# Optimization experiments

Hardware: AMD Instinct MI355X
Metric: run time of the kernel (lower is better)

## Reference

```python
import jax, jax.numpy as jnp
import numpy as np

DIM = 1024
SEQ = 32768
BATCH = 1
MIN_ACTIVE = 0.01
MAX_ACTIVE = 0.1
KMAX = int(MAX_ACTIVE * DIM) + 1  # static upper bound on dynamic k (<= 102)
EPS = 1e-6


def setup_inputs() -> dict:
    key = jax.random.key(0)
    ks = jax.random.split(key, 7)
    h = DIM // 8
    s = 0.02
    return {
        "x": jax.random.normal(ks[0], (BATCH, SEQ, DIM), jnp.float32),
        # complexity_net: Linear(dim, dim//8) -> GELU -> Linear(dim//8, 1) -> Sigmoid
        "w1": jax.random.normal(ks[1], (DIM, h), jnp.float32) * s,
        "b1": jnp.zeros((h,), jnp.float32),
        "w2": jax.random.normal(ks[2], (h, 1), jnp.float32) * s,
        "b2": jnp.zeros((1,), jnp.float32),
        # gate_net: Linear(dim, dim)
        "wg": jax.random.normal(ks[3], (DIM, DIM), jnp.float32) * s,
        "bg": jnp.zeros((DIM,), jnp.float32),
        # running stats (eval mode: used for normalization, not updated)
        "running_mean": jax.random.normal(ks[4], (DIM,), jnp.float32) * 0.1,
        "running_var": jax.random.uniform(ks[5], (DIM,), jnp.float32, minval=0.5, maxval=1.5),
    }


def reference(x, w1, b1, w2, b2, wg, bg, running_mean, running_var):
    # complexity from seq-mean pooled features -> scalar in (0,1)
    pooled = x.mean(axis=1, keepdims=True)                      # (B,1,D)
    hid = jax.nn.gelu(pooled @ w1 + b1, approximate=False)      # torch GELU is exact erf
    complexity = jax.nn.sigmoid(hid @ w2 + b2)                  # (B,1,1)
    active_ratio = MIN_ACTIVE + (MAX_ACTIVE - MIN_ACTIVE) * complexity
    # torch .int() truncates; clamp(min=1). B==1 so k is effectively scalar.
    k = jnp.clip((active_ratio * DIM).astype(jnp.int32), 1, KMAX)  # (B,1,1)

    importance = jnp.abs(x @ wg + bg)                           # (B,S,D)
    importance = (importance - running_mean) / (jnp.sqrt(running_var) + EPS)

    # dynamic-k topk via static-KMAX top_k + threshold at the k-th largest value
    topk_vals, _ = jax.lax.top_k(importance, KMAX)              # (B,S,KMAX)
    idx = jnp.broadcast_to((k - 1).astype(jnp.int32), (x.shape[0], x.shape[1], 1))
    kth = jnp.take_along_axis(topk_vals, idx, axis=-1)          # (B,S,1)
    mask = (importance >= kth).astype(x.dtype)                  # (B,S,D), non-differentiable
    mask = jax.lax.stop_gradient(mask)

    # straight-through combine: forward = x*mask, backward passes grad to all of x
    sparse_x = x * mask + (x - jax.lax.stop_gradient(x)) * (1.0 - mask)

    complexity_mean = complexity.mean()
    active_ratio_mean = active_ratio.mean()
    active_neurons = k.astype(jnp.float32).mean()
    return sparse_x, complexity_mean, active_ratio_mean, active_neurons
```

## Files before the change

### kernel.cpp

```cpp
#include <hip/hip_runtime.h>
#include <cstdint>
#include <cstddef>

#define SEQ 32768
#define DIM 1024
#define HID 128
#define KMAXV 103

using f4 = __attribute__((ext_vector_type(4))) float;

__global__ __launch_bounds__(256) void pool_partial(const float* __restrict__ x,
                                                    double* __restrict__ part) {
    const int b = blockIdx.x;
    const int t = threadIdx.x;
    const int r0 = b * 128;
    double s0 = 0.0, s1 = 0.0, s2 = 0.0, s3 = 0.0;
    for (int r = 0; r < 128; ++r) {
        const float* row = x + (size_t)(r0 + r) * DIM;
        s0 += (double)row[t];
        s1 += (double)row[t + 256];
        s2 += (double)row[t + 512];
        s3 += (double)row[t + 768];
    }
    double* p = part + (size_t)b * DIM;
    p[t] = s0; p[t + 256] = s1; p[t + 512] = s2; p[t + 768] = s3;
}

__global__ __launch_bounds__(1024) void tiny_net(const double* __restrict__ part,
                                                 const float* __restrict__ w1,
                                                 const float* __restrict__ b1,
                                                 const float* __restrict__ w2,
                                                 const float* __restrict__ b2,
                                                 float* __restrict__ out_scalars,
                                                 int* __restrict__ kout) {
    __shared__ double pooled[DIM];
    __shared__ double hidv[HID];
    const int t = threadIdx.x;

    double s = 0.0;
    for (int b = 0; b < 256; ++b) s += part[(size_t)b * DIM + t];
    pooled[t] = s / (double)SEQ;
    __syncthreads();

    if (t < HID) {
        double h = (double)b1[t];
        for (int d = 0; d < DIM; ++d) h += pooled[d] * (double)w1[d * HID + t];
        h = 0.5 * h * (1.0 + erf(h * 0.70710678118654752440));
        hidv[t] = h;
    }
    __syncthreads();

    if (t == 0) {
        double z = (double)b2[0];
        for (int j = 0; j < HID; ++j) z += hidv[j] * (double)w2[j];
        double c = 1.0 / (1.0 + exp(-z));
        double ar = 0.01 + 0.09 * c;
        int k = (int)(ar * (double)DIM);
        if (k < 1) k = 1;
        if (k > KMAXV) k = KMAXV;
        out_scalars[0] = (float)c;
        out_scalars[1] = (float)ar;
        out_scalars[2] = (float)k;
        *kout = k;
    }
}

#define BM 16
#define CBLOCK 512

__global__ __launch_bounds__(CBLOCK, 4) void gate_kernel(const float* __restrict__ x,
                                                         const float* __restrict__ wg,
                                                         const float* __restrict__ bg,
                                                         const float* __restrict__ rm,
                                                         const float* __restrict__ rv,
                                                         const int* __restrict__ kptr,
                                                         float* __restrict__ out) {
    __shared__ float xs[BM][DIM];
    float (*selbuf)[DIM] = (float (*)[DIM])xs;

    const int t = threadIdx.x;
    const int c4 = (t & 255) << 2;
    const int rg = t >> 8;
    const int row0 = blockIdx.x * BM;

    {
        const f4* xg = (const f4*)(x + (size_t)row0 * DIM);
        f4* xl = (f4*)xs;
        for (int i = t; i < BM * (DIM / 4); i += CBLOCK) xl[i] = xg[i];
    }
    __syncthreads();

    float dot[8][4];
#pragma unroll
    for (int m = 0; m < 8; ++m)
#pragma unroll
        for (int j = 0; j < 4; ++j) dot[m][j] = 0.0f;

    const int pb[4] = {0, 384, 704, 1024};
    const float* xrow = &xs[rg * 8][0];
    const float* wbase = wg + c4;

    for (int p = 0; p < 3; ++p) {
        float pacc[8][4];
#pragma unroll
        for (int m = 0; m < 8; ++m)
#pragma unroll
            for (int j = 0; j < 4; ++j) pacc[m][j] = 0.0f;

        for (int kk0 = pb[p]; kk0 < pb[p + 1]; kk0 += 4) {
            const f4 wq0 = *(const f4*)(wbase + (size_t)(kk0 + 0) * DIM);
            const f4 wq1 = *(const f4*)(wbase + (size_t)(kk0 + 1) * DIM);
            const f4 wq2 = *(const f4*)(wbase + (size_t)(kk0 + 2) * DIM);
            const f4 wq3 = *(const f4*)(wbase + (size_t)(kk0 + 3) * DIM);
#pragma unroll
            for (int m = 0; m < 8; ++m) {
                const f4 xv = *(const f4*)(xrow + m * DIM + kk0);
#pragma unroll
                for (int j = 0; j < 4; ++j) {
                    float a = pacc[m][j];
                    a = fmaf(xv[0], wq0[j], a);
                    a = fmaf(xv[1], wq1[j], a);
                    a = fmaf(xv[2], wq2[j], a);
                    a = fmaf(xv[3], wq3[j], a);
                    pacc[m][j] = a;
                }
            }
        }
#pragma unroll
        for (int m = 0; m < 8; ++m)
#pragma unroll
            for (int j = 0; j < 4; ++j) dot[m][j] += pacc[m][j];
    }

    const f4 vbg = *(const f4*)(bg + c4);
    const f4 vrm = *(const f4*)(rm + c4);
    const f4 vrv = *(const f4*)(rv + c4);
    f4 vden;
#pragma unroll
    for (int j = 0; j < 4; ++j) vden[j] = sqrtf(vrv[j]) + 1e-6f;

    f4 imp[8];
#pragma unroll
    for (int m = 0; m < 8; ++m)
#pragma unroll
        for (int j = 0; j < 4; ++j) {
            const float v = fabsf(dot[m][j] + vbg[j]);
            imp[m][j] = (v - vrm[j]) / vden[j];
        }

    int kval = *kptr;
    if (kval < 1) kval = 1;
    if (kval > DIM) kval = DIM;

    for (int ch = 0; ch < 2; ++ch) {
        __syncthreads();
        if (rg == ch) {
#pragma unroll
            for (int m = 0; m < 8; ++m)
                *(f4*)(&selbuf[m][c4]) = imp[m];
        }
        __syncthreads();

        const int w = t >> 6;
        const int l = t & 63;
        const size_t srow = (size_t)(row0 + ch * 8 + w);

        unsigned keys[16];
#pragma unroll
        for (int j = 0; j < 4; ++j) {
            const f4 v = *(const f4*)(&selbuf[w][4 * l + 256 * j]);
#pragma unroll
            for (int i = 0; i < 4; ++i) {
                const unsigned u = __float_as_uint(v[i]);
                keys[j * 4 + i] = (u & 0x80000000u) ? ~u : (u | 0x80000000u);
            }
        }

        unsigned pref = 0u;
        for (int b = 31; b >= 0; --b) {
            const unsigned tt = pref | (1u << b);
            int cnt = 0;
#pragma unroll
            for (int j = 0; j < 16; ++j) cnt += (keys[j] >= tt) ? 1 : 0;
#pragma unroll
            for (int off = 32; off >= 1; off >>= 1) cnt += __shfl_xor(cnt, off, 64);
            if (cnt >= kval) pref = tt;
        }

        const float* xr = x + srow * DIM;
        float* orow = out + srow * DIM;
#pragma unroll
        for (int j = 0; j < 4; ++j) {
            const f4 xv = *(const f4*)(xr + 4 * l + 256 * j);
            f4 o;
#pragma unroll
            for (int i = 0; i < 4; ++i) o[i] = (keys[j * 4 + i] >= pref) ? xv[i] : 0.0f;
            *(f4*)(orow + 4 * l + 256 * j) = o;
        }
    }
}

extern "C" void kernel_launch(void* const* d_in, const int* in_sizes, int n_in,
                              void* d_out, int out_size, void* d_ws, size_t ws_size,
                              hipStream_t stream) {
    const float* x  = (const float*)d_in[0];
    const float* w1 = (const float*)d_in[1];
    const float* b1 = (const float*)d_in[2];
    const float* w2 = (const float*)d_in[3];
    const float* b2 = (const float*)d_in[4];
    const float* wg = (const float*)d_in[5];
    const float* bg = (const float*)d_in[6];
    const float* rm = (const float*)d_in[7];
    const float* rv = (const float*)d_in[8];
    float* out = (float*)d_out;

    double* part = (double*)d_ws;
    int* kptr = (int*)((char*)d_ws + (size_t)256 * DIM * sizeof(double));

    pool_partial<<<256, 256, 0, stream>>>(x, part);
    tiny_net<<<1, 1024, 0, stream>>>(part, w1, b1, w2, b2,
                                     out + (size_t)SEQ * DIM, kptr);
    gate_kernel<<<SEQ / BM, CBLOCK, 0, stream>>>(x, wg, bg, rm, rv, kptr, out);
}
```

Before: 1.153 ms.

## Remap gate GEMM threads to a 16-row by 2-column register tile

Each thread now computes 16 rows by 2 columns of the gate matmul instead of 8 rows by 4 columns. The whole block therefore reads each weight column once rather than twice, which halves global/L2 weight traffic per block. The cost is twice as many LDS reads of x (broadcast across threads) and narrower float2 weight loads. The min-blocks-per-CU hint is also dropped from launch bounds, which gives the compiler more registers but may lower occupancy.

```diff
diff --git a/kernel.cpp b/kernel.cpp
--- a/kernel.cpp
+++ b/kernel.cpp
@@ -8,6 +8,7 @@
 #define KMAXV 103
 
 using f4 = __attribute__((ext_vector_type(4))) float;
+using f2 = __attribute__((ext_vector_type(2))) float;
 
 __global__ __launch_bounds__(256) void pool_partial(const float* __restrict__ x,
                                                     double* __restrict__ part) {
@@ -68,19 +69,18 @@
 #define BM 16
 #define CBLOCK 512
 
-__global__ __launch_bounds__(CBLOCK, 4) void gate_kernel(const float* __restrict__ x,
-                                                         const float* __restrict__ wg,
-                                                         const float* __restrict__ bg,
-                                                         const float* __restrict__ rm,
-                                                         const float* __restrict__ rv,
-                                                         const int* __restrict__ kptr,
-                                                         float* __restrict__ out) {
+__global__ __launch_bounds__(CBLOCK) void gate_kernel(const float* __restrict__ x,
+                                                      const float* __restrict__ wg,
+                                                      const float* __restrict__ bg,
+                                                      const float* __restrict__ rm,
+                                                      const float* __restrict__ rv,
+                                                      const int* __restrict__ kptr,
+                                                      float* __restrict__ out) {
     __shared__ float xs[BM][DIM];
     float (*selbuf)[DIM] = (float (*)[DIM])xs;
 
     const int t = threadIdx.x;
-    const int c4 = (t & 255) << 2;
-    const int rg = t >> 8;
+    const int c2 = t << 1;
     const int row0 = blockIdx.x * BM;
 
     {
@@ -90,60 +90,50 @@
     }
     __syncthreads();
 
-    float dot[8][4];
-#pragma unroll
-    for (int m = 0; m < 8; ++m)
-#pragma unroll
-        for (int j = 0; j < 4; ++j) dot[m][j] = 0.0f;
+    float dot[16][2];
+#pragma unroll
+    for (int m = 0; m < 16; ++m) { dot[m][0] = 0.0f; dot[m][1] = 0.0f; }
 
     const int pb[4] = {0, 384, 704, 1024};
-    const float* xrow = &xs[rg * 8][0];
-    const float* wbase = wg + c4;
+    const float* wbase = wg + c2;
 
     for (int p = 0; p < 3; ++p) {
-        float pacc[8][4];
-#pragma unroll
-        for (int m = 0; m < 8; ++m)
-#pragma unroll
-            for (int j = 0; j < 4; ++j) pacc[m][j] = 0.0f;
+        float pacc[16][2];
+#pragma unroll
+        for (int m = 0; m < 16; ++m) { pacc[m][0] = 0.0f; pacc[m][1] = 0.0f; }
 
         for (int kk0 = pb[p]; kk0 < pb[p + 1]; kk0 += 4) {
-            const f4 wq0 = *(const f4*)(wbase + (size_t)(kk0 + 0) * DIM);
-            const f4 wq1 = *(const f4*)(wbase + (size_t)(kk0 + 1) * DIM);
-            const f4 wq2 = *(const f4*)(wbase + (size_t)(kk0 + 2) * DIM);
-            const f4 wq3 = *(const f4*)(wbase + (size_t)(kk0 + 3) * DIM);
-#pragma unroll
-            for (int m = 0; m < 8; ++m) {
-                const f4 xv = *(const f4*)(xrow + m * DIM + kk0);
-#pragma unroll
-                for (int j = 0; j < 4; ++j) {
-                    float a = pacc[m][j];
-                    a = fmaf(xv[0], wq0[j], a);
-                    a = fmaf(xv[1], wq1[j], a);
-                    a = fmaf(xv[2], wq2[j], a);
-                    a = fmaf(xv[3], wq3[j], a);
-                    pacc[m][j] = a;
-                }
+            const f2 w0 = *(const f2*)(wbase + (size_t)(kk0 + 0) * DIM);
+            const f2 w1v = *(const f2*)(wbase + (size_t)(kk0 + 1) * DIM);
+            const f2 w2v = *(const f2*)(wbase + (size_t)(kk0 + 2) * DIM);
+            const f2 w3v = *(const f2*)(wbase + (size_t)(kk0 + 3) * DIM);
+#pragma unroll
+            for (int m = 0; m < 16; ++m) {
+                const f4 xv = *(const f4*)(&xs[m][kk0]);
+                float a0 = pacc[m][0], a1 = pacc[m][1];
+                a0 = fmaf(xv[0], w0[0], a0);  a1 = fmaf(xv[0], w0[1], a1);
+                a0 = fmaf(xv[1], w1v[0], a0); a1 = fmaf(xv[1], w1v[1], a1);
+                a0 = fmaf(xv[2], w2v[0], a0); a1 = fmaf(xv[2], w2v[1], a1);
+                a0 = fmaf(xv[3], w3v[0], a0); a1 = fmaf(xv[3], w3v[1], a1);
+                pacc[m][0] = a0; pacc[m][1] = a1;
             }
         }
 #pragma unroll
-        for (int m = 0; m < 8; ++m)
-#pragma unroll
-            for (int j = 0; j < 4; ++j) dot[m][j] += pacc[m][j];
-    }
-
-    const f4 vbg = *(const f4*)(bg + c4);
-    const f4 vrm = *(const f4*)(rm + c4);
-    const f4 vrv = *(const f4*)(rv + c4);
-    f4 vden;
-#pragma unroll
-    for (int j = 0; j < 4; ++j) vden[j] = sqrtf(vrv[j]) + 1e-6f;
-
-    f4 imp[8];
-#pragma unroll
-    for (int m = 0; m < 8; ++m)
-#pragma unroll
-        for (int j = 0; j < 4; ++j) {
+        for (int m = 0; m < 16; ++m) { dot[m][0] += pacc[m][0]; dot[m][1] += pacc[m][1]; }
+    }
+
+    const f2 vbg = *(const f2*)(bg + c2);
+    const f2 vrm = *(const f2*)(rm + c2);
+    const f2 vrv = *(const f2*)(rv + c2);
+    f2 vden;
+    vden[0] = sqrtf(vrv[0]) + 1e-6f;
+    vden[1] = sqrtf(vrv[1]) + 1e-6f;
+
+    float imp[16][2];
+#pragma unroll
+    for (int m = 0; m < 16; ++m)
+#pragma unroll
+        for (int j = 0; j < 2; ++j) {
             const float v = fabsf(dot[m][j] + vbg[j]);
             imp[m][j] = (v - vrm[j]) / vden[j];
         }
@@ -154,10 +144,10 @@
 
     for (int ch = 0; ch < 2; ++ch) {
         __syncthreads();
-        if (rg == ch) {
-#pragma unroll
-            for (int m = 0; m < 8; ++m)
-                *(f4*)(&selbuf[m][c4]) = imp[m];
+#pragma unroll
+        for (int m = 0; m < 8; ++m) {
+            f2 v; v[0] = imp[ch * 8 + m][0]; v[1] = imp[ch * 8 + m][1];
+            *(f2*)(&selbuf[m][c2]) = v;
         }
         __syncthreads();
 
```

After: 1.802 ms. 1.56x slower.
